# Kernel optimization log

Measured on AMD Instinct MI355X. Metric: run time of the kernel, lower is better.

The kernel has to match this reference:

```python
import jax, jax.numpy as jnp
import numpy as np

# Model constants (match init_kwargs)
DIM = 1024
INTER = 1024
E = 32          # n_routed_experts
K = 4           # n_activated_experts
G = 8           # n_expert_groups
LG = 4          # n_limited_groups
ROUTE_SCALE = 1.0
CAP_FACTOR = 1.25
B, S = 4, 2048


def setup_inputs() -> dict:
    key = jax.random.key(0)
    ks = jax.random.split(key, 9)
    sd = DIM ** -0.5
    si = INTER ** -0.5
    x = jax.random.normal(ks[0], (B, S, DIM), jnp.float32)
    wg = jax.random.normal(ks[1], (E, DIM), jnp.float32) * sd          # gate weight [E, dim]
    w1 = jax.random.normal(ks[2], (E, DIM, INTER), jnp.float32) * sd   # stacked expert w1
    w3 = jax.random.normal(ks[3], (E, DIM, INTER), jnp.float32) * sd   # stacked expert w3
    w2 = jax.random.normal(ks[4], (E, INTER, DIM), jnp.float32) * si   # stacked expert w2
    sw1 = jax.random.normal(ks[5], (DIM, INTER), jnp.float32) * sd     # shared SwiGLU
    sw3 = jax.random.normal(ks[6], (DIM, INTER), jnp.float32) * sd
    sw2 = jax.random.normal(ks[7], (INTER, DIM), jnp.float32) * si
    return dict(x=x, wg=wg, w1=w1, w2=w2, w3=w3, sw1=sw1, sw2=sw2, sw3=sw3)


def _gate(xf, wg):
    # Group-limited top-k gating (router_noise_std=0, temperature=1.0).
    logits = xf @ wg.T                                  # [N, E]
    scores = jax.nn.softmax(logits, axis=-1)
    sg = scores.reshape(-1, G, E // G)                  # [N, G, E/G]
    group_scores = sg.max(axis=-1)                      # [N, G]
    _, gtop = jax.lax.top_k(group_scores, LG)           # [N, LG]
    keep_g = jnp.sum(jax.nn.one_hot(gtop, G, dtype=jnp.float32), axis=1) > 0  # [N, G]
    masked = jnp.where(keep_g[:, :, None], sg, -jnp.inf).reshape(-1, E)
    _, idx = jax.lax.top_k(masked, K)                   # [N, K]
    w = jnp.take_along_axis(scores, idx, axis=1)        # gather from ORIGINAL scores
    w = w / (w.sum(-1, keepdims=True) + 1e-9) * ROUTE_SCALE
    return w.astype(xf.dtype), idx


def _forward(x, wg, w1, w2, w3, sw1, sw2, sw3):
    shape = x.shape
    xf = x.reshape(-1, DIM)
    N = xf.shape[0]
    cap = max(1, int(CAP_FACTOR * N * K / E))           # per-expert capacity (static)
    w, idx = _gate(xf, wg)

    # --- dispatch with capacity: position of each (token, slot) within its expert,
    # counted in row-major (token-major) order == torch.where order in the original.
    fe = idx.reshape(-1)                                # [N*K] expert ids
    oh = jax.nn.one_hot(fe, E, dtype=jnp.int32)         # [N*K, E]
    pos = (jnp.cumsum(oh, axis=0) * oh).sum(-1) - 1     # rank within expert
    keep = pos < cap
    dest = jnp.where(keep, fe * cap + pos, E * cap)     # dropped -> pad slot
    tok = jnp.arange(N * K, dtype=jnp.int32) // K
    buf_tok = jnp.full((E * cap + 1,), N, jnp.int32).at[dest].set(tok)[:-1]       # [E*cap]
    buf_w = jnp.zeros((E * cap + 1,), x.dtype).at[dest].set(w.reshape(-1))[:-1]   # [E*cap]

    # --- grouped gather-GEMM-scatter (pad row of zeros for empty slots)
    xp = jnp.concatenate([xf, jnp.zeros((1, DIM), x.dtype)], axis=0)
    xe = xp[buf_tok].reshape(E, cap, DIM)
    h = jax.nn.silu(jnp.einsum('ecd,edh->ech', xe, w1)) * jnp.einsum('ecd,edh->ech', xe, w3)
    out = jnp.einsum('ech,ehd->ecd', h, w2) * buf_w.reshape(E, cap, 1)
    y = jnp.zeros((N + 1, DIM), x.dtype).at[buf_tok].add(out.reshape(E * cap, DIM))[:N]

    # --- shared experts (SwiGLU with inter dim == inter_dim via expansion formula)
    z = (jax.nn.silu(xf @ sw1) * (xf @ sw3)) @ sw2
    return (y + z).reshape(shape)


def reference(x, wg, w1, w2, w3, sw1, sw2, sw3):
    return _forward(x, wg, w1, w2, w3, sw1, sw2, sw3)
```

## Files before the change

kernel.cpp:

```cpp
#include <hip/hip_runtime.h>
#include <stdint.h>

#define NTOK 8192
#define CAP  1280
#define NEXP 32

typedef __bf16 bf16x8 __attribute__((ext_vector_type(8)));
typedef float f32x4 __attribute__((ext_vector_type(4)));
typedef unsigned short u16;

__device__ __forceinline__ u16 f2bf(float f) {
  unsigned u = __builtin_bit_cast(unsigned, f);
  u = (u + 0x7fffu + ((u >> 16) & 1u)) >> 16;
  return (u16)u;
}
__device__ __forceinline__ float bf2f(u16 h) {
  return __builtin_bit_cast(float, ((unsigned)h) << 16);
}

__device__ __forceinline__ void gload16(const void* g, void* l) {
  __builtin_amdgcn_global_load_lds(
      (const __attribute__((address_space(1))) void*)g,
      (__attribute__((address_space(3))) void*)l, 16, 0, 0);
}

#define VM0 asm volatile("s_waitcnt vmcnt(0)" ::: "memory")

__global__ __launch_bounds__(256) void conv_x_kernel(const float* __restrict__ in,
                                                     u16* __restrict__ out) {
  int i = blockIdx.x * 256 + threadIdx.x;
  float4 v = reinterpret_cast<const float4*>(in)[i];
  uint2 o;
  o.x = (unsigned)f2bf(v.x) | ((unsigned)f2bf(v.y) << 16);
  o.y = (unsigned)f2bf(v.z) | ((unsigned)f2bf(v.w) << 16);
  reinterpret_cast<uint2*>(out)[i] = o;
}

__global__ __launch_bounds__(256) void tconv_all_kernel(
    const float* __restrict__ w1, const float* __restrict__ w3,
    const float* __restrict__ w2, const float* __restrict__ sw1,
    const float* __restrict__ sw3, const float* __restrict__ sw2,
    u16* __restrict__ w1t, u16* __restrict__ w3t, u16* __restrict__ w2t,
    u16* __restrict__ sw1t, u16* __restrict__ sw3t, u16* __restrict__ sw2t) {
  __shared__ float tile[32][33];
  const int z = blockIdx.z;
  const float* src;
  u16* dst;
  if (z < 32)      { src = w1 + (size_t)z * 1048576;        dst = w1t + (size_t)z * 1048576; }
  else if (z < 64) { src = w3 + (size_t)(z - 32) * 1048576; dst = w3t + (size_t)(z - 32) * 1048576; }
  else if (z < 96) { src = w2 + (size_t)(z - 64) * 1048576; dst = w2t + (size_t)(z - 64) * 1048576; }
  else if (z == 96){ src = sw1; dst = sw1t; }
  else if (z == 97){ src = sw3; dst = sw3t; }
  else             { src = sw2; dst = sw2t; }
  int r0 = blockIdx.x * 32, c0 = blockIdx.y * 32;
  int tid = threadIdx.x;
#pragma unroll
  for (int i = 0; i < 4; ++i) {
    int t = tid + i * 256, r = t >> 5, c = t & 31;
    tile[r][c] = src[(size_t)(r0 + r) * 1024 + (c0 + c)];
  }
  __syncthreads();
#pragma unroll
  for (int i = 0; i < 4; ++i) {
    int t = tid + i * 256, cc = t >> 5, rr = t & 31;
    dst[(size_t)(c0 + cc) * 1024 + (r0 + rr)] = f2bf(tile[rr][cc]);
  }
}

__global__ __launch_bounds__(256) void gate_kernel(const float* __restrict__ x,
                                                   const float* __restrict__ wg,
                                                   int* __restrict__ gidx,
                                                   float* __restrict__ gw) {
  const int t = blockIdx.x;
  __shared__ float xl[1024];
  __shared__ float logits[32];
  const int tid = threadIdx.x;
  reinterpret_cast<float4*>(xl)[tid] = reinterpret_cast<const float4*>(x + (size_t)t * 1024)[tid];
  __syncthreads();
  const int e = tid >> 3, p = tid & 7;
  const float4* wrow = reinterpret_cast<const float4*>(wg + (size_t)e * 1024);
  const float4* xv4 = reinterpret_cast<const float4*>(xl);
  float s = 0.f;
#pragma unroll
  for (int i = 0; i < 32; ++i) {
    int c = p + 8 * i;
    float4 xv = xv4[c];
    float4 wv = wrow[c];
    s += xv.x * wv.x + xv.y * wv.y + xv.z * wv.z + xv.w * wv.w;
  }
  s += __shfl_xor(s, 1);
  s += __shfl_xor(s, 2);
  s += __shfl_xor(s, 4);
  if (p == 0) logits[e] = s;
  __syncthreads();
  if (tid == 0) {
    float m = logits[0];
#pragma unroll
    for (int i = 1; i < 32; ++i) m = fmaxf(m, logits[i]);
    float sum = 0.f;
#pragma unroll
    for (int i = 0; i < 32; ++i) sum += expf(logits[i] - m);
    float gm[8];
#pragma unroll
    for (int g = 0; g < 8; ++g) {
      float v = logits[4 * g];
      v = fmaxf(v, logits[4 * g + 1]);
      v = fmaxf(v, logits[4 * g + 2]);
      v = fmaxf(v, logits[4 * g + 3]);
      gm[g] = v;
    }
    unsigned gkeep = 0;
    for (int it = 0; it < 4; ++it) {
      float best = -3.4e38f; int bg = 0;
#pragma unroll
      for (int g = 0; g < 8; ++g) {
        bool ok = !((gkeep >> g) & 1u);
        if (ok && gm[g] > best) { best = gm[g]; bg = g; }
      }
      gkeep |= 1u << bg;
    }
    unsigned allow = 0;
#pragma unroll
    for (int g = 0; g < 8; ++g)
      if ((gkeep >> g) & 1u) allow |= 0xFu << (4 * g);
    unsigned taken = 0;
    float wsum = 0.f;
    int ids[4]; float wv[4];
    for (int sIt = 0; sIt < 4; ++sIt) {
      float best = -3.4e38f; int be = 0;
#pragma unroll
      for (int i = 0; i < 32; ++i) {
        bool ok = ((allow >> i) & 1u) && !((taken >> i) & 1u);
        float v = logits[i];
        if (ok && v > best) { best = v; be = i; }
      }
      taken |= 1u << be;
      ids[sIt] = be;
      float wq = expf(logits[be] - m) / sum;
      wv[sIt] = wq;
      wsum += wq;
    }
    float inv = 1.f / (wsum + 1e-9f);
#pragma unroll
    for (int sIt = 0; sIt < 4; ++sIt) {
      gidx[t * 4 + sIt] = ids[sIt];
      gw[t * 4 + sIt] = wv[sIt] * inv;
    }
  }
}

__global__ __launch_bounds__(256) void initbuf_kernel(int* __restrict__ bt, float* __restrict__ bw) {
  int i = blockIdx.x * 256 + threadIdx.x;
  if (i < NEXP * CAP) { bt[i] = -1; bw[i] = 0.f; }
}

__global__ __launch_bounds__(1024) void rank_kernel(const int* __restrict__ gidx,
                                                    const float* __restrict__ gw,
                                                    int* __restrict__ buf_tok,
                                                    float* __restrict__ buf_w,
                                                    int* __restrict__ cnt,
                                                    int* __restrict__ tslot) {
  const int e = blockIdx.x;
  const int tid = threadIdx.x, wid = tid >> 6, lane = tid & 63;
  __shared__ int wtot[16];
  int base = 0;
  for (int j0 = 0; j0 < NTOK * 4; j0 += 1024) {
    int j = j0 + tid;
    bool match = (gidx[j] == e);
    unsigned long long mb = __ballot(match);
    if (lane == 0) wtot[wid] = __popcll(mb);
    __syncthreads();
    int woff = 0, btot = 0;
#pragma unroll
    for (int w = 0; w < 16; ++w) {
      int c = wtot[w];
      if (w < wid) woff += c;
      btot += c;
    }
    if (match) {
      int pos = base + woff + __popcll(mb & ((1ull << lane) - 1ull));
      if (pos < CAP) {
        buf_tok[e * CAP + pos] = j >> 2;
        buf_w[e * CAP + pos] = gw[j];
        tslot[j] = e * CAP + pos;
      } else {
        tslot[j] = -1;
      }
    }
    base += btot;
    __syncthreads();
  }
  if (tid == 0) cnt[e] = (base < CAP) ? base : CAP;
}

__global__ __launch_bounds__(512, 4) void up8_kernel(const u16* __restrict__ X,
                                                     const u16* __restrict__ w1t,
                                                     const u16* __restrict__ w3t,
                                                     const u16* __restrict__ sw1t,
                                                     const u16* __restrict__ sw3t,
                                                     u16* __restrict__ hs,
                                                     u16* __restrict__ he,
                                                     const int* __restrict__ btok,
                                                     const int* __restrict__ cnt) {
  extern __shared__ __align__(16) u16 lds_raw[];
  const int tid = threadIdx.x, wid = tid >> 6, lane = tid & 63;
  const int bid = blockIdx.x;
  const int xcd = bid & 7, off = bid >> 3;
  bool expert;
  int mt, nt, e = 0;
  const u16 *B1, *B3;
  u16* H;
  if (off < 320) {
    expert = true;
    int id = xcd * 320 + off;
    e = id / 80;
    int r = id % 80;
    mt = r % 5;
    nt = r / 5;
    if (mt * 256 >= cnt[e]) return;
    B1 = w1t + ((size_t)e << 20);
    B3 = w3t + ((size_t)e << 20);
    H = he + (size_t)(e * CAP + mt * 256) * 1024;
  } else {
    expert = false;
    int id = xcd * 64 + (off - 320);
    mt = id % 32;
    nt = id / 32;
    B1 = sw1t;
    B3 = sw3t;
    H = hs + (size_t)mt * 256 * 1024;
  }
  const int wr = wid >> 1, wc = wid & 1;
  const int fr = lane & 15, fw = lane >> 4;

  const int srow = tid >> 2;
  const int slot4 = tid & 3;
  const int sw = ((slot4 ^ ((srow >> 1) & 3)) << 3);

  const u16* aP[2];
#pragma unroll
  for (int j = 0; j < 2; ++j) {
    int row = mt * 256 + j * 128 + srow;
    int grow;
    if (expert) {
      int t0 = btok[e * CAP + row];
      grow = (t0 < 0) ? 0 : t0;
    } else {
      grow = row;
    }
    aP[j] = X + (size_t)grow * 1024 + sw;
  }
  const u16* bP;
  {
    int q = srow >> 5, s = srow & 31;
    const u16* base = (s < 16) ? B1 : B3;
    bP = base + (size_t)(nt * 64 + q * 16 + (s & 15)) * 1024 + sw;
  }

  auto stage = [&](int c) {
    u16* dA = lds_raw + (c & 1) * 12288 + wid * 512;
    const int g = c * 32;
    gload16(aP[0] + g, dA);
    gload16(aP[1] + g, dA + 4096);
    gload16(bP + g, dA + 8192);
  };

  const int swz = ((fw ^ ((fr >> 1) & 3)) << 3);
  const u16* aRd = lds_raw + (wr * 64 + fr) * 32 + swz;
  const u16* bRd = lds_raw + 8192 + (wc * 64 + fr) * 32 + swz;

  f32x4 acc[4][4] = {};

  stage(0);
  VM0;
  __builtin_amdgcn_s_barrier();

  for (int c = 0; c < 32; ++c) {
    const int off16 = (c & 1) * 12288;
    bf16x8 av[4], bv[4];
#pragma unroll
    for (int m = 0; m < 4; ++m)
      av[m] = *reinterpret_cast<const bf16x8*>(aRd + off16 + m * 512);
#pragma unroll
    for (int n = 0; n < 4; ++n)
      bv[n] = *reinterpret_cast<const bf16x8*>(bRd + off16 + n * 512);
    if (c < 31) stage(c + 1);
    __builtin_amdgcn_s_setprio(1);
#pragma unroll
    for (int m = 0; m < 4; ++m)
#pragma unroll
      for (int n = 0; n < 4; ++n)
        acc[m][n] = __builtin_amdgcn_mfma_f32_16x16x32_bf16(av[m], bv[n], acc[m][n], 0, 0, 0);
    __builtin_amdgcn_s_setprio(0);
    if (c < 31) {
      VM0;
      __builtin_amdgcn_s_barrier();
    }
  }

  const int row0 = wr * 64 + fw * 4;
  const int col0 = nt * 64 + wc * 32;
#pragma unroll
  for (int m = 0; m < 4; ++m)
#pragma unroll
    for (int k = 0; k < 2; ++k)
#pragma unroll
      for (int ri = 0; ri < 4; ++ri) {
        float v1 = acc[m][2 * k][ri];
        float v3 = acc[m][2 * k + 1][ri];
        float h = (v1 / (1.f + __expf(-v1))) * v3;
        H[(size_t)(row0 + m * 16 + ri) * 1024 + col0 + k * 16 + fr] = f2bf(h);
      }
}

__global__ __launch_bounds__(512, 4) void down8_kernel(const u16* __restrict__ hs,
                                                       const u16* __restrict__ he,
                                                       const u16* __restrict__ sB,
                                                       const u16* __restrict__ eB,
                                                       float* __restrict__ Out,
                                                       u16* __restrict__ OutB,
                                                       const float* __restrict__ bw,
                                                       const int* __restrict__ cnt) {
  extern __shared__ __align__(16) u16 lds_raw[];
  const int tid = threadIdx.x, wid = tid >> 6, lane = tid & 63;
  const int bid = blockIdx.x;
  const int xcd = bid & 7, off = bid >> 3;
  bool expert;
  int mt, nt, e = 0;
  const u16 *Asrc, *Bsrc;
  if (off < 160) {
    expert = true;
    int id = xcd * 160 + off;
    e = id / 40;
    int r = id % 40;
    mt = r % 5;
    nt = r / 5;
    if (mt * 256 >= cnt[e]) return;
    Asrc = he + (size_t)e * CAP * 1024;
    Bsrc = eB + ((size_t)e << 20);
  } else {
    expert = false;
    int id = xcd * 32 + (off - 160);
    mt = id % 32;
    nt = id / 32;
    Asrc = hs;
    Bsrc = sB;
  }
  const int wr = wid >> 1, wc = wid & 1;
  const int fr = lane & 15, fw = lane >> 4;

  const int srow = tid >> 2;
  const int slot4 = tid & 3;
  const int sw = ((slot4 ^ ((srow >> 1) & 3)) << 3);

  const u16* aP[2];
#pragma unroll
  for (int j = 0; j < 2; ++j)
    aP[j] = Asrc + (size_t)(mt * 256 + j * 128 + srow) * 1024 + sw;
  const u16* bP = Bsrc + (size_t)(nt * 128 + srow) * 1024 + sw;

  auto stage = [&](int c) {
    u16* dA = lds_raw + (c & 1) * 12288 + wid * 512;
    const int g = c * 32;
    gload16(aP[0] + g, dA);
    gload16(aP[1] + g, dA + 4096);
    gload16(bP + g, dA + 8192);
  };

  const int swz = ((fw ^ ((fr >> 1) & 3)) << 3);
  const u16* aRd = lds_raw + (wr * 64 + fr) * 32 + swz;
  const u16* bRd = lds_raw + 8192 + (wc * 64 + fr) * 32 + swz;

  f32x4 acc[4][4] = {};

  stage(0);
  VM0;
  __builtin_amdgcn_s_barrier();

  for (int c = 0; c < 32; ++c) {
    const int off16 = (c & 1) * 12288;
    bf16x8 av[4], bv[4];
#pragma unroll
    for (int m = 0; m < 4; ++m)
      av[m] = *reinterpret_cast<const bf16x8*>(aRd + off16 + m * 512);
#pragma unroll
    for (int n = 0; n < 4; ++n)
      bv[n] = *reinterpret_cast<const bf16x8*>(bRd + off16 + n * 512);
    if (c < 31) stage(c + 1);
    __builtin_amdgcn_s_setprio(1);
#pragma unroll
    for (int m = 0; m < 4; ++m)
#pragma unroll
      for (int n = 0; n < 4; ++n)
        acc[m][n] = __builtin_amdgcn_mfma_f32_16x16x32_bf16(av[m], bv[n], acc[m][n], 0, 0, 0);
    __builtin_amdgcn_s_setprio(0);
    if (c < 31) {
      VM0;
      __builtin_amdgcn_s_barrier();
    }
  }

  const int orow0 = mt * 256 + wr * 64 + fw * 4;
  const int ocol0 = nt * 128 + wc * 64;
  if (expert) {
#pragma unroll
    for (int m = 0; m < 4; ++m)
#pragma unroll
      for (int ri = 0; ri < 4; ++ri) {
        int row = orow0 + m * 16 + ri;
        int slot = e * CAP + (row - mt * 256) + mt * 256;
        float wgt = bw[e * CAP + row];
#pragma unroll
        for (int n = 0; n < 4; ++n)
          OutB[(size_t)(e * CAP + row) * 1024 + ocol0 + n * 16 + fr] = f2bf(acc[m][n][ri] * wgt);
        (void)slot;
      }
  } else {
#pragma unroll
    for (int m = 0; m < 4; ++m)
#pragma unroll
      for (int ri = 0; ri < 4; ++ri) {
        int row = orow0 + m * 16 + ri;
#pragma unroll
        for (int n = 0; n < 4; ++n)
          Out[(size_t)row * 1024 + ocol0 + n * 16 + fr] = acc[m][n][ri];
      }
  }
}

__global__ __launch_bounds__(256) void combine_kernel(const u16* __restrict__ oe,
                                                      const int* __restrict__ tslot,
                                                      float* __restrict__ out) {
  const int t = blockIdx.x;
  const int c = threadIdx.x;
  int s0 = tslot[t * 4 + 0], s1 = tslot[t * 4 + 1];
  int s2 = tslot[t * 4 + 2], s3 = tslot[t * 4 + 3];
  float4 v = reinterpret_cast<float4*>(out + (size_t)t * 1024)[c];
  auto addsl = [&](int s) {
    if (s >= 0) {
      uint2 q = reinterpret_cast<const uint2*>(oe + (size_t)s * 1024)[c];
      v.x += bf2f((u16)(q.x & 0xffff));
      v.y += bf2f((u16)(q.x >> 16));
      v.z += bf2f((u16)(q.y & 0xffff));
      v.w += bf2f((u16)(q.y >> 16));
    }
  };
  addsl(s0); addsl(s1); addsl(s2); addsl(s3);
  reinterpret_cast<float4*>(out + (size_t)t * 1024)[c] = v;
}

extern "C" void kernel_launch(void* const* d_in, const int* in_sizes, int n_in,
                              void* d_out, int out_size, void* d_ws, size_t ws_size,
                              hipStream_t stream) {
  const float* x   = (const float*)d_in[0];
  const float* wg  = (const float*)d_in[1];
  const float* w1  = (const float*)d_in[2];
  const float* w2  = (const float*)d_in[3];
  const float* w3  = (const float*)d_in[4];
  const float* sw1 = (const float*)d_in[5];
  const float* sw2 = (const float*)d_in[6];
  const float* sw3 = (const float*)d_in[7];
  float* out = (float*)d_out;

  char* p = (char*)d_ws;
  auto alloc = [&](size_t bytes) {
    char* q = p;
    p += (bytes + 255) & ~(size_t)255;
    return q;
  };
  u16* xb   = (u16*)alloc((size_t)NTOK * 1024 * 2);
  u16* w1t  = (u16*)alloc((size_t)NEXP * 1024 * 1024 * 2);
  u16* w3t  = (u16*)alloc((size_t)NEXP * 1024 * 1024 * 2);
  u16* w2t  = (u16*)alloc((size_t)NEXP * 1024 * 1024 * 2);
  u16* sw1t = (u16*)alloc((size_t)1024 * 1024 * 2);
  u16* sw3t = (u16*)alloc((size_t)1024 * 1024 * 2);
  u16* sw2t = (u16*)alloc((size_t)1024 * 1024 * 2);
  u16* hs   = (u16*)alloc((size_t)NTOK * 1024 * 2);
  u16* he   = (u16*)alloc((size_t)NEXP * CAP * 1024 * 2);
  int*   gidx = (int*)alloc((size_t)NTOK * 4 * 4);
  float* gww  = (float*)alloc((size_t)NTOK * 4 * 4);
  int*   btok = (int*)alloc((size_t)NEXP * CAP * 4);
  float* bww  = (float*)alloc((size_t)NEXP * CAP * 4);
  int*   cnt  = (int*)alloc((size_t)NEXP * 4);
  int*   tslot= (int*)alloc((size_t)NTOK * 4 * 4);
  u16* oe = w1t;

  conv_x_kernel<<<NTOK * 1024 / 1024, 256, 0, stream>>>(x, xb);
  tconv_all_kernel<<<dim3(32, 32, 99), 256, 0, stream>>>(w1, w3, w2, sw1, sw3, sw2,
                                                         w1t, w3t, w2t, sw1t, sw3t, sw2t);
  gate_kernel<<<NTOK, 256, 0, stream>>>(x, wg, gidx, gww);
  initbuf_kernel<<<(NEXP * CAP + 255) / 256, 256, 0, stream>>>(btok, bww);
  rank_kernel<<<NEXP, 1024, 0, stream>>>(gidx, gww, btok, bww, cnt, tslot);
  up8_kernel<<<3072, 512, 49152, stream>>>(xb, w1t, w3t, sw1t, sw3t, hs, he, btok, cnt);
  down8_kernel<<<1536, 512, 49152, stream>>>(hs, he, sw2t, w2t, out, oe, bww, cnt);
  combine_kernel<<<NTOK, 256, 0, stream>>>(oe, tslot, out);
}
```

Before: 578.2 us.

## Triple-buffer LDS staging in up and down GEMM kernels with partial vmcnt waits

```diff
diff --git a/kernel.cpp b/kernel.cpp
--- a/kernel.cpp
+++ b/kernel.cpp
@@ -24,6 +24,7 @@
       (__attribute__((address_space(3))) void*)l, 16, 0, 0);
 }
 
+#define VM3 asm volatile("s_waitcnt vmcnt(3)" ::: "memory")
 #define VM0 asm volatile("s_waitcnt vmcnt(0)" ::: "memory")
 
 __global__ __launch_bounds__(256) void conv_x_kernel(const float* __restrict__ in,
@@ -257,8 +258,8 @@
     bP = base + (size_t)(nt * 64 + q * 16 + (s & 15)) * 1024 + sw;
   }
 
-  auto stage = [&](int c) {
-    u16* dA = lds_raw + (c & 1) * 12288 + wid * 512;
+  auto stage = [&](int c, int sl) {
+    u16* dA = lds_raw + sl * 12288 + wid * 512;
     const int g = c * 32;
     gload16(aP[0] + g, dA);
     gload16(aP[1] + g, dA + 4096);
@@ -271,20 +272,22 @@
 
   f32x4 acc[4][4] = {};
 
-  stage(0);
-  VM0;
+  stage(0, 0);
+  stage(1, 1);
+  VM3;
   __builtin_amdgcn_s_barrier();
 
+  int sl = 0, slw = 2;
   for (int c = 0; c < 32; ++c) {
-    const int off16 = (c & 1) * 12288;
+    const int offL = sl * 12288;
     bf16x8 av[4], bv[4];
 #pragma unroll
     for (int m = 0; m < 4; ++m)
-      av[m] = *reinterpret_cast<const bf16x8*>(aRd + off16 + m * 512);
+      av[m] = *reinterpret_cast<const bf16x8*>(aRd + offL + m * 512);
 #pragma unroll
     for (int n = 0; n < 4; ++n)
-      bv[n] = *reinterpret_cast<const bf16x8*>(bRd + off16 + n * 512);
-    if (c < 31) stage(c + 1);
+      bv[n] = *reinterpret_cast<const bf16x8*>(bRd + offL + n * 512);
+    if (c < 30) stage(c + 2, slw);
     __builtin_amdgcn_s_setprio(1);
 #pragma unroll
     for (int m = 0; m < 4; ++m)
@@ -292,10 +295,15 @@
       for (int n = 0; n < 4; ++n)
         acc[m][n] = __builtin_amdgcn_mfma_f32_16x16x32_bf16(av[m], bv[n], acc[m][n], 0, 0, 0);
     __builtin_amdgcn_s_setprio(0);
-    if (c < 31) {
+    if (c < 30) {
+      VM3;
+      __builtin_amdgcn_s_barrier();
+    } else if (c == 30) {
       VM0;
       __builtin_amdgcn_s_barrier();
     }
+    sl = (sl == 2) ? 0 : sl + 1;
+    slw = (slw == 2) ? 0 : slw + 1;
   }
 
   const int row0 = wr * 64 + fw * 4;
@@ -359,8 +367,8 @@
     aP[j] = Asrc + (size_t)(mt * 256 + j * 128 + srow) * 1024 + sw;
   const u16* bP = Bsrc + (size_t)(nt * 128 + srow) * 1024 + sw;
 
-  auto stage = [&](int c) {
-    u16* dA = lds_raw + (c & 1) * 12288 + wid * 512;
+  auto stage = [&](int c, int sl) {
+    u16* dA = lds_raw + sl * 12288 + wid * 512;
     const int g = c * 32;
     gload16(aP[0] + g, dA);
     gload16(aP[1] + g, dA + 4096);
@@ -373,20 +381,22 @@
 
   f32x4 acc[4][4] = {};
 
-  stage(0);
-  VM0;
+  stage(0, 0);
+  stage(1, 1);
+  VM3;
   __builtin_amdgcn_s_barrier();
 
+  int sl = 0, slw = 2;
   for (int c = 0; c < 32; ++c) {
-    const int off16 = (c & 1) * 12288;
+    const int offL = sl * 12288;
     bf16x8 av[4], bv[4];
 #pragma unroll
     for (int m = 0; m < 4; ++m)
-      av[m] = *reinterpret_cast<const bf16x8*>(aRd + off16 + m * 512);
+      av[m] = *reinterpret_cast<const bf16x8*>(aRd + offL + m * 512);
 #pragma unroll
     for (int n = 0; n < 4; ++n)
-      bv[n] = *reinterpret_cast<const bf16x8*>(bRd + off16 + n * 512);
-    if (c < 31) stage(c + 1);
+      bv[n] = *reinterpret_cast<const bf16x8*>(bRd + offL + n * 512);
+    if (c < 30) stage(c + 2, slw);
     __builtin_amdgcn_s_setprio(1);
 #pragma unroll
     for (int m = 0; m < 4; ++m)
@@ -394,10 +404,15 @@
       for (int n = 0; n < 4; ++n)
         acc[m][n] = __builtin_amdgcn_mfma_f32_16x16x32_bf16(av[m], bv[n], acc[m][n], 0, 0, 0);
     __builtin_amdgcn_s_setprio(0);
-    if (c < 31) {
+    if (c < 30) {
+      VM3;
+      __builtin_amdgcn_s_barrier();
+    } else if (c == 30) {
       VM0;
       __builtin_amdgcn_s_barrier();
     }
+    sl = (sl == 2) ? 0 : sl + 1;
+    slw = (slw == 2) ? 0 : slw + 1;
   }
 
   const int orow0 = mt * 256 + wr * 64 + fw * 4;
@@ -408,12 +423,10 @@
 #pragma unroll
       for (int ri = 0; ri < 4; ++ri) {
         int row = orow0 + m * 16 + ri;
-        int slot = e * CAP + (row - mt * 256) + mt * 256;
         float wgt = bw[e * CAP + row];
 #pragma unroll
         for (int n = 0; n < 4; ++n)
           OutB[(size_t)(e * CAP + row) * 1024 + ocol0 + n * 16 + fr] = f2bf(acc[m][n][ri] * wgt);
-        (void)slot;
       }
   } else {
 #pragma unroll
@@ -491,7 +504,7 @@
   gate_kernel<<<NTOK, 256, 0, stream>>>(x, wg, gidx, gww);
   initbuf_kernel<<<(NEXP * CAP + 255) / 256, 256, 0, stream>>>(btok, bww);
   rank_kernel<<<NEXP, 1024, 0, stream>>>(gidx, gww, btok, bww, cnt, tslot);
-  up8_kernel<<<3072, 512, 49152, stream>>>(xb, w1t, w3t, sw1t, sw3t, hs, he, btok, cnt);
-  down8_kernel<<<1536, 512, 49152, stream>>>(hs, he, sw2t, w2t, out, oe, bww, cnt);
+  up8_kernel<<<3072, 512, 73728, stream>>>(xb, w1t, w3t, sw1t, sw3t, hs, he, btok, cnt);
+  down8_kernel<<<1536, 512, 73728, stream>>>(hs, he, sw2t, w2t, out, oe, bww, cnt);
   combine_kernel<<<NTOK, 256, 0, stream>>>(oe, tslot, out);
 }
```

Measured after the change: 567.4 us. No clear change (-1.9%).

## Enlarge GEMM tiles to 256x256 with BK=64 and interleaved LDS-read/MFMA pipeline

Applied to the files above, without the earlier changes.

```diff
diff --git a/kernel.cpp b/kernel.cpp
--- a/kernel.cpp
+++ b/kernel.cpp
@@ -23,8 +23,6 @@
       (const __attribute__((address_space(1))) void*)g,
       (__attribute__((address_space(3))) void*)l, 16, 0, 0);
 }
-
-#define VM0 asm volatile("s_waitcnt vmcnt(0)" ::: "memory")
 
 __global__ __launch_bounds__(256) void conv_x_kernel(const float* __restrict__ in,
                                                      u16* __restrict__ out) {
@@ -193,7 +191,48 @@
   if (tid == 0) cnt[e] = (base < CAP) ? base : CAP;
 }
 
-__global__ __launch_bounds__(512, 4) void up8_kernel(const u16* __restrict__ X,
+
+#define RD_A(dst, PI, MH, KS)                                                     \
+  _Pragma("unroll") for (int i_ = 0; i_ < 4; ++i_)                                \
+      dst[i_] = *reinterpret_cast<const bf16x8*>(                                 \
+          ((KS) ? aB1 : aB0) + (PI) * 16384 + (MH) * 4096 + i_ * 1024);
+
+#define RD_B(dst, PI, KS)                                                         \
+  _Pragma("unroll") for (int n_ = 0; n_ < 4; ++n_)                                \
+      dst[n_] = *reinterpret_cast<const bf16x8*>(                                 \
+          ((KS) ? bB1 : bB0) + (PI) * 16384 + n_ * 1024);
+
+#define QUAD(MH, AV, BV)                                                          \
+  __builtin_amdgcn_s_setprio(1);                                                  \
+  _Pragma("unroll") for (int i_ = 0; i_ < 4; ++i_)                                \
+    _Pragma("unroll") for (int n_ = 0; n_ < 4; ++n_)                              \
+        acc[(MH) * 4 + i_][n_] = __builtin_amdgcn_mfma_f32_16x16x32_bf16(         \
+            AV[i_], BV[n_], acc[(MH) * 4 + i_][n_], 0, 0, 0);                     \
+  __builtin_amdgcn_s_setprio(0);
+
+#define KSYNC                                                                     \
+  asm volatile("s_waitcnt lgkmcnt(0)" ::: "memory");                              \
+  __builtin_amdgcn_sched_barrier(0);                                              \
+  asm volatile("s_waitcnt vmcnt(0)" ::: "memory");                                \
+  __builtin_amdgcn_s_barrier();                                                   \
+  __builtin_amdgcn_sched_barrier(0);
+
+#define KTILE(PI, KT, STG, NXT)                                                   \
+  {                                                                               \
+    RD_A(av1, PI, 1, 0)                                                           \
+    QUAD(0, av0, bv0)                                                             \
+    RD_A(av0, PI, 0, 1)                                                           \
+    RD_B(bv1, PI, 1)                                                              \
+    QUAD(1, av1, bv0)                                                             \
+    RD_A(av1, PI, 1, 1)                                                           \
+    QUAD(0, av0, bv1)                                                             \
+    KSYNC                                                                         \
+    if (NXT) { RD_A(av0, 1 - (PI), 0, 0) RD_B(bv0, 1 - (PI), 0) }                 \
+    if (STG) stageK((KT) + 2, PI);                                                \
+    QUAD(1, av1, bv1)                                                             \
+  }
+
+__global__ __launch_bounds__(512, 2) void up8_kernel(const u16* __restrict__ X,
                                                      const u16* __restrict__ w1t,
                                                      const u16* __restrict__ w3t,
                                                      const u16* __restrict__ sw1t,
@@ -202,7 +241,7 @@
                                                      u16* __restrict__ he,
                                                      const int* __restrict__ btok,
                                                      const int* __restrict__ cnt) {
-  extern __shared__ __align__(16) u16 lds_raw[];
+  extern __shared__ __align__(16) u16 lds[];
   const int tid = threadIdx.x, wid = tid >> 6, lane = tid & 63;
   const int bid = blockIdx.x;
   const int xcd = bid & 7, off = bid >> 3;
@@ -210,11 +249,11 @@
   int mt, nt, e = 0;
   const u16 *B1, *B3;
   u16* H;
-  if (off < 320) {
+  if (off < 160) {
     expert = true;
-    int id = xcd * 320 + off;
-    e = id / 80;
-    int r = id % 80;
+    int id = xcd * 160 + off;
+    e = id / 40;
+    int r = id % 40;
     mt = r % 5;
     nt = r / 5;
     if (mt * 256 >= cnt[e]) return;
@@ -223,24 +262,22 @@
     H = he + (size_t)(e * CAP + mt * 256) * 1024;
   } else {
     expert = false;
-    int id = xcd * 64 + (off - 320);
+    int id = xcd * 32 + (off - 160);
     mt = id % 32;
     nt = id / 32;
     B1 = sw1t;
     B3 = sw3t;
     H = hs + (size_t)mt * 256 * 1024;
   }
-  const int wr = wid >> 1, wc = wid & 1;
+  const int wr = wid >> 2, wc = wid & 3;
   const int fr = lane & 15, fw = lane >> 4;
 
-  const int srow = tid >> 2;
-  const int slot4 = tid & 3;
-  const int sw = ((slot4 ^ ((srow >> 1) & 3)) << 3);
-
-  const u16* aP[2];
-#pragma unroll
-  for (int j = 0; j < 2; ++j) {
-    int row = mt * 256 + j * 128 + srow;
+  const int sr = tid >> 3;
+  const int colw = ((tid & 7) ^ (sr & 7)) << 3;
+  const u16* aP[4];
+#pragma unroll
+  for (int j = 0; j < 4; ++j) {
+    int row = mt * 256 + j * 64 + sr;
     int grow;
     if (expert) {
       int t0 = btok[e * CAP + row];
@@ -248,72 +285,64 @@
     } else {
       grow = row;
     }
-    aP[j] = X + (size_t)grow * 1024 + sw;
-  }
-  const u16* bP;
+    aP[j] = X + (size_t)grow * 1024 + colw;
+  }
+  const u16* bP[4];
   {
-    int q = srow >> 5, s = srow & 31;
-    const u16* base = (s < 16) ? B1 : B3;
-    bP = base + (size_t)(nt * 64 + q * 16 + (s & 15)) * 1024 + sw;
-  }
-
-  auto stage = [&](int c) {
-    u16* dA = lds_raw + (c & 1) * 12288 + wid * 512;
-    const int g = c * 32;
-    gload16(aP[0] + g, dA);
-    gload16(aP[1] + g, dA + 4096);
-    gload16(bP + g, dA + 8192);
+    int q = sr >> 5, t = sr & 31;
+    const u16* base = (t < 16) ? B1 : B3;
+#pragma unroll
+    for (int j = 0; j < 4; ++j)
+      bP[j] = base + (size_t)(nt * 128 + j * 32 + q * 16 + (t & 15)) * 1024 + colw;
+  }
+
+  auto stageK = [&](int kt, int pi) {
+    const int g = kt * 64;
+    u16* dA = lds + pi * 16384 + wid * 512;
+    u16* dB = lds + 32768 + pi * 16384 + wid * 512;
+#pragma unroll
+    for (int j = 0; j < 4; ++j) gload16(aP[j] + g, dA + j * 4096);
+#pragma unroll
+    for (int j = 0; j < 4; ++j) gload16(bP[j] + g, dB + j * 4096);
   };
 
-  const int swz = ((fw ^ ((fr >> 1) & 3)) << 3);
-  const u16* aRd = lds_raw + (wr * 64 + fr) * 32 + swz;
-  const u16* bRd = lds_raw + 8192 + (wc * 64 + fr) * 32 + swz;
-
-  f32x4 acc[4][4] = {};
-
-  stage(0);
-  VM0;
+  const int S0 = fw ^ (fr & 7);
+  const u16* aB0 = lds + (wr * 128 + fr) * 64 + S0 * 8;
+  const u16* aB1 = lds + (wr * 128 + fr) * 64 + (S0 ^ 4) * 8;
+  const u16* bB0 = lds + 32768 + (wc * 64 + fr) * 64 + S0 * 8;
+  const u16* bB1 = lds + 32768 + (wc * 64 + fr) * 64 + (S0 ^ 4) * 8;
+
+  f32x4 acc[8][4] = {};
+  bf16x8 av0[4], av1[4], bv0[4], bv1[4];
+
+  stageK(0, 0);
+  stageK(1, 1);
+  asm volatile("s_waitcnt vmcnt(8)" ::: "memory");
   __builtin_amdgcn_s_barrier();
-
-  for (int c = 0; c < 32; ++c) {
-    const int off16 = (c & 1) * 12288;
-    bf16x8 av[4], bv[4];
-#pragma unroll
-    for (int m = 0; m < 4; ++m)
-      av[m] = *reinterpret_cast<const bf16x8*>(aRd + off16 + m * 512);
-#pragma unroll
-    for (int n = 0; n < 4; ++n)
-      bv[n] = *reinterpret_cast<const bf16x8*>(bRd + off16 + n * 512);
-    if (c < 31) stage(c + 1);
-    __builtin_amdgcn_s_setprio(1);
-#pragma unroll
-    for (int m = 0; m < 4; ++m)
-#pragma unroll
-      for (int n = 0; n < 4; ++n)
-        acc[m][n] = __builtin_amdgcn_mfma_f32_16x16x32_bf16(av[m], bv[n], acc[m][n], 0, 0, 0);
-    __builtin_amdgcn_s_setprio(0);
-    if (c < 31) {
-      VM0;
-      __builtin_amdgcn_s_barrier();
-    }
-  }
-
-  const int row0 = wr * 64 + fw * 4;
-  const int col0 = nt * 64 + wc * 32;
-#pragma unroll
-  for (int m = 0; m < 4; ++m)
-#pragma unroll
-    for (int k = 0; k < 2; ++k)
+  RD_A(av0, 0, 0, 0)
+  RD_B(bv0, 0, 0)
+
+  for (int kt = 0; kt < 16; kt += 2) {
+    KTILE(0, kt, kt <= 12, true)
+    KTILE(1, kt + 1, kt <= 12, kt + 1 < 15)
+  }
+
+  const int row0 = wr * 128 + fw * 4;
+  const int hc0 = nt * 128 + wc * 32 + fr;
+#pragma unroll
+  for (int m = 0; m < 8; ++m)
+#pragma unroll
+    for (int q = 0; q < 2; ++q)
 #pragma unroll
       for (int ri = 0; ri < 4; ++ri) {
-        float v1 = acc[m][2 * k][ri];
-        float v3 = acc[m][2 * k + 1][ri];
+        float v1 = acc[m][2 * q][ri];
+        float v3 = acc[m][2 * q + 1][ri];
         float h = (v1 / (1.f + __expf(-v1))) * v3;
-        H[(size_t)(row0 + m * 16 + ri) * 1024 + col0 + k * 16 + fr] = f2bf(h);
+        H[(size_t)(row0 + m * 16 + ri) * 1024 + hc0 + q * 16] = f2bf(h);
       }
 }
 
-__global__ __launch_bounds__(512, 4) void down8_kernel(const u16* __restrict__ hs,
+__global__ __launch_bounds__(512, 2) void down8_kernel(const u16* __restrict__ hs,
                                                        const u16* __restrict__ he,
                                                        const u16* __restrict__ sB,
                                                        const u16* __restrict__ eB,
@@ -321,18 +350,18 @@
                                                        u16* __restrict__ OutB,
                                                        const float* __restrict__ bw,
                                                        const int* __restrict__ cnt) {
-  extern __shared__ __align__(16) u16 lds_raw[];
+  extern __shared__ __align__(16) u16 lds[];
   const int tid = threadIdx.x, wid = tid >> 6, lane = tid & 63;
   const int bid = blockIdx.x;
   const int xcd = bid & 7, off = bid >> 3;
   bool expert;
   int mt, nt, e = 0;
   const u16 *Asrc, *Bsrc;
-  if (off < 160) {
+  if (off < 80) {
     expert = true;
-    int id = xcd * 160 + off;
-    e = id / 40;
-    int r = id % 40;
+    int id = xcd * 80 + off;
+    e = id / 20;
+    int r = id % 20;
     mt = r % 5;
     nt = r / 5;
     if (mt * 256 >= cnt[e]) return;
@@ -340,90 +369,78 @@
     Bsrc = eB + ((size_t)e << 20);
   } else {
     expert = false;
-    int id = xcd * 32 + (off - 160);
+    int id = xcd * 16 + (off - 80);
     mt = id % 32;
     nt = id / 32;
     Asrc = hs;
     Bsrc = sB;
   }
-  const int wr = wid >> 1, wc = wid & 1;
+  const int wr = wid >> 2, wc = wid & 3;
   const int fr = lane & 15, fw = lane >> 4;
 
-  const int srow = tid >> 2;
-  const int slot4 = tid & 3;
-  const int sw = ((slot4 ^ ((srow >> 1) & 3)) << 3);
-
-  const u16* aP[2];
-#pragma unroll
-  for (int j = 0; j < 2; ++j)
-    aP[j] = Asrc + (size_t)(mt * 256 + j * 128 + srow) * 1024 + sw;
-  const u16* bP = Bsrc + (size_t)(nt * 128 + srow) * 1024 + sw;
-
-  auto stage = [&](int c) {
-    u16* dA = lds_raw + (c & 1) * 12288 + wid * 512;
-    const int g = c * 32;
-    gload16(aP[0] + g, dA);
-    gload16(aP[1] + g, dA + 4096);
-    gload16(bP + g, dA + 8192);
+  const int sr = tid >> 3;
+  const int colw = ((tid & 7) ^ (sr & 7)) << 3;
+  const u16* aP[4];
+  const u16* bP[4];
+#pragma unroll
+  for (int j = 0; j < 4; ++j) {
+    aP[j] = Asrc + (size_t)(mt * 256 + j * 64 + sr) * 1024 + colw;
+    bP[j] = Bsrc + (size_t)(nt * 256 + j * 64 + sr) * 1024 + colw;
+  }
+
+  auto stageK = [&](int kt, int pi) {
+    const int g = kt * 64;
+    u16* dA = lds + pi * 16384 + wid * 512;
+    u16* dB = lds + 32768 + pi * 16384 + wid * 512;
+#pragma unroll
+    for (int j = 0; j < 4; ++j) gload16(aP[j] + g, dA + j * 4096);
+#pragma unroll
+    for (int j = 0; j < 4; ++j) gload16(bP[j] + g, dB + j * 4096);
   };
 
-  const int swz = ((fw ^ ((fr >> 1) & 3)) << 3);
-  const u16* aRd = lds_raw + (wr * 64 + fr) * 32 + swz;
-  const u16* bRd = lds_raw + 8192 + (wc * 64 + fr) * 32 + swz;
-
-  f32x4 acc[4][4] = {};
-
-  stage(0);
-  VM0;
+  const int S0 = fw ^ (fr & 7);
+  const u16* aB0 = lds + (wr * 128 + fr) * 64 + S0 * 8;
+  const u16* aB1 = lds + (wr * 128 + fr) * 64 + (S0 ^ 4) * 8;
+  const u16* bB0 = lds + 32768 + (wc * 64 + fr) * 64 + S0 * 8;
+  const u16* bB1 = lds + 32768 + (wc * 64 + fr) * 64 + (S0 ^ 4) * 8;
+
+  f32x4 acc[8][4] = {};
+  bf16x8 av0[4], av1[4], bv0[4], bv1[4];
+
+  stageK(0, 0);
+  stageK(1, 1);
+  asm volatile("s_waitcnt vmcnt(8)" ::: "memory");
   __builtin_amdgcn_s_barrier();
-
-  for (int c = 0; c < 32; ++c) {
-    const int off16 = (c & 1) * 12288;
-    bf16x8 av[4], bv[4];
-#pragma unroll
-    for (int m = 0; m < 4; ++m)
-      av[m] = *reinterpret_cast<const bf16x8*>(aRd + off16 + m * 512);
-#pragma unroll
-    for (int n = 0; n < 4; ++n)
-      bv[n] = *reinterpret_cast<const bf16x8*>(bRd + off16 + n * 512);
-    if (c < 31) stage(c + 1);
-    __builtin_amdgcn_s_setprio(1);
-#pragma unroll
-    for (int m = 0; m < 4; ++m)
-#pragma unroll
-      for (int n = 0; n < 4; ++n)
-        acc[m][n] = __builtin_amdgcn_mfma_f32_16x16x32_bf16(av[m], bv[n], acc[m][n], 0, 0, 0);
-    __builtin_amdgcn_s_setprio(0);
-    if (c < 31) {
-      VM0;
-      __builtin_amdgcn_s_barrier();
-    }
-  }
-
-  const int orow0 = mt * 256 + wr * 64 + fw * 4;
-  const int ocol0 = nt * 128 + wc * 64;
+  RD_A(av0, 0, 0, 0)
+  RD_B(bv0, 0, 0)
+
+  for (int kt = 0; kt < 16; kt += 2) {
+    KTILE(0, kt, kt <= 12, true)
+    KTILE(1, kt + 1, kt <= 12, kt + 1 < 15)
+  }
+
+  const int orow0 = mt * 256 + wr * 128 + fw * 4;
+  const int oc0 = nt * 256 + wc * 64 + fr;
   if (expert) {
 #pragma unroll
-    for (int m = 0; m < 4; ++m)
+    for (int m = 0; m < 8; ++m)
 #pragma unroll
       for (int ri = 0; ri < 4; ++ri) {
         int row = orow0 + m * 16 + ri;
-        int slot = e * CAP + (row - mt * 256) + mt * 256;
         float wgt = bw[e * CAP + row];
 #pragma unroll
         for (int n = 0; n < 4; ++n)
-          OutB[(size_t)(e * CAP + row) * 1024 + ocol0 + n * 16 + fr] = f2bf(acc[m][n][ri] * wgt);
-        (void)slot;
+          OutB[(size_t)(e * CAP + row) * 1024 + oc0 + n * 16] = f2bf(acc[m][n][ri] * wgt);
       }
   } else {
 #pragma unroll
-    for (int m = 0; m < 4; ++m)
+    for (int m = 0; m < 8; ++m)
 #pragma unroll
       for (int ri = 0; ri < 4; ++ri) {
         int row = orow0 + m * 16 + ri;
 #pragma unroll
         for (int n = 0; n < 4; ++n)
-          Out[(size_t)row * 1024 + ocol0 + n * 16 + fr] = acc[m][n][ri];
+          Out[(size_t)row * 1024 + oc0 + n * 16] = acc[m][n][ri];
       }
   }
 }
@@ -491,7 +508,7 @@
   gate_kernel<<<NTOK, 256, 0, stream>>>(x, wg, gidx, gww);
   initbuf_kernel<<<(NEXP * CAP + 255) / 256, 256, 0, stream>>>(btok, bww);
   rank_kernel<<<NEXP, 1024, 0, stream>>>(gidx, gww, btok, bww, cnt, tslot);
-  up8_kernel<<<3072, 512, 49152, stream>>>(xb, w1t, w3t, sw1t, sw3t, hs, he, btok, cnt);
-  down8_kernel<<<1536, 512, 49152, stream>>>(hs, he, sw2t, w2t, out, oe, bww, cnt);
+  up8_kernel<<<1536, 512, 131072, stream>>>(xb, w1t, w3t, sw1t, sw3t, hs, he, btok, cnt);
+  down8_kernel<<<768, 512, 131072, stream>>>(hs, he, sw2t, w2t, out, oe, bww, cnt);
   combine_kernel<<<NTOK, 256, 0, stream>>>(oe, tslot, out);
 }
```

New measurement: 884.2 us. 1.53x slower.
